# Kernel tuning notes

Hardware: AMD Instinct MI355X
Metric: run time of the kernel (lower is better)

The kernel has to match this reference:

```python
import jax, jax.numpy as jnp
import numpy as np

TEMPERATURE = 0.5
EPS = 1e-12  # torch F.normalize eps


def _l2_normalize(x, eps=EPS):
    n = jnp.linalg.norm(x, axis=1, keepdims=True)
    return x / jnp.maximum(n, eps)


def setup_inputs() -> dict:
    key = jax.random.key(0)
    k1, k2 = jax.random.split(key)
    B, D = 4096, 512
    return {
        "polyline_embs": jax.random.normal(k1, (B, D), dtype=jnp.float32),
        "c_embs": jax.random.normal(k2, (B, D), dtype=jnp.float32),
    }


def reference(polyline_embs, c_embs):
    b = polyline_embs.shape[0]
    # double-normalization in the original (F.normalize then cosine_similarity)
    # is idempotent on unit vectors, so sim = Z @ Z^T with Z unit-normalized.
    z = _l2_normalize(jnp.concatenate([polyline_embs, c_embs], axis=0))  # [2B, D]
    sim = z @ z.T  # [2B, 2B] cosine similarity
    # positives: diag offsets +B and -B
    idx = jnp.arange(b)
    sim_ij = sim[idx, idx + b]
    sim_ji = sim[idx + b, idx]
    positives = jnp.concatenate([sim_ij, sim_ji], axis=0)  # [2B]
    nominator = jnp.exp(positives / TEMPERATURE)
    mask = 1.0 - jnp.eye(2 * b, dtype=sim.dtype)
    denominator = jnp.sum(mask * jnp.exp(sim / TEMPERATURE), axis=1)  # [2B]
    all_losses = -jnp.log(nominator / denominator)
    return jnp.sum(all_losses) / (2 * b)
```

## Files before the change

### kernel.cpp

```cpp
#include <hip/hip_runtime.h>
#include <hip/hip_bf16.h>

#define B_ROWS 4096
#define D_DIM  512
#define N_ROWS 8192
#define BM 128
#define BN 128
#define BKB 128
#define NBLK (N_ROWS / BM)
#define NPAIR (NBLK * (NBLK + 1) / 2)

typedef float f32x4 __attribute__((ext_vector_type(4)));
typedef int   v4i   __attribute__((ext_vector_type(4)));
typedef int   v8i   __attribute__((ext_vector_type(8)));

__device__ __forceinline__ float dpp_xor1_add(float v) {
    return v + __int_as_float(__builtin_amdgcn_mov_dpp(
        __float_as_int(v), 0xB1, 0xf, 0xf, true));
}
__device__ __forceinline__ float dpp_xor2_add(float v) {
    return v + __int_as_float(__builtin_amdgcn_mov_dpp(
        __float_as_int(v), 0x4E, 0xf, 0xf, true));
}
__device__ __forceinline__ float dpp_ror4_add(float v) {
    return v + __int_as_float(__builtin_amdgcn_mov_dpp(
        __float_as_int(v), 0x124, 0xf, 0xf, true));
}
__device__ __forceinline__ float dpp_ror8_add(float v) {
    return v + __int_as_float(__builtin_amdgcn_mov_dpp(
        __float_as_int(v), 0x128, 0xf, 0xf, true));
}

__global__ __launch_bounds__(256) void prep_kernel(
    const float* __restrict__ poly, const float* __restrict__ cemb,
    unsigned char* __restrict__ Z, float* __restrict__ row_sum,
    float* __restrict__ pos, unsigned int* __restrict__ counter)
{
    const int wave = threadIdx.x >> 6;
    const int lane = threadIdx.x & 63;
    const int r = blockIdx.x * 4 + wave;

    const float4* prow = (const float4*)(poly + (size_t)r * D_DIM) + lane * 2;
    const float4* crow = (const float4*)(cemb + (size_t)r * D_DIM) + lane * 2;
    const float4 p0 = prow[0], p1 = prow[1];
    const float4 c0 = crow[0], c1 = crow[1];

    float ssp = p0.x*p0.x + p0.y*p0.y + p0.z*p0.z + p0.w*p0.w
              + p1.x*p1.x + p1.y*p1.y + p1.z*p1.z + p1.w*p1.w;
    float ssc = c0.x*c0.x + c0.y*c0.y + c0.z*c0.z + c0.w*c0.w
              + c1.x*c1.x + c1.y*c1.y + c1.z*c1.z + c1.w*c1.w;
    float dt  = p0.x*c0.x + p0.y*c0.y + p0.z*c0.z + p0.w*c0.w
              + p1.x*c1.x + p1.y*c1.y + p1.z*c1.z + p1.w*c1.w;

    #pragma unroll
    for (int m = 1; m < 64; m <<= 1) {
        ssp += __shfl_xor(ssp, m);
        ssc += __shfl_xor(ssc, m);
        dt  += __shfl_xor(dt,  m);
    }

    const float sp = 1.0f / fmaxf(sqrtf(ssp), 1e-12f);
    const float sc = 1.0f / fmaxf(sqrtf(ssc), 1e-12f);

    int2 zp, zc;
    zp.x = __builtin_amdgcn_cvt_pk_fp8_f32(p0.x*sp, p0.y*sp, 0, false)
         | (__builtin_amdgcn_cvt_pk_fp8_f32(p0.z*sp, p0.w*sp, 0, false) << 16);
    zp.y = __builtin_amdgcn_cvt_pk_fp8_f32(p1.x*sp, p1.y*sp, 0, false)
         | (__builtin_amdgcn_cvt_pk_fp8_f32(p1.z*sp, p1.w*sp, 0, false) << 16);
    zc.x = __builtin_amdgcn_cvt_pk_fp8_f32(c0.x*sc, c0.y*sc, 0, false)
         | (__builtin_amdgcn_cvt_pk_fp8_f32(c0.z*sc, c0.w*sc, 0, false) << 16);
    zc.y = __builtin_amdgcn_cvt_pk_fp8_f32(c1.x*sc, c1.y*sc, 0, false)
         | (__builtin_amdgcn_cvt_pk_fp8_f32(c1.z*sc, c1.w*sc, 0, false) << 16);

    *(int2*)(Z + (size_t)r * D_DIM + lane * 8)            = zp;
    *(int2*)(Z + (size_t)(r + B_ROWS) * D_DIM + lane * 8) = zc;

    if (lane == 0) {
        pos[r] = dt * sp * sc;
        row_sum[2 * r]     = 0.0f;
        row_sum[2 * r + 1] = 0.0f;
        if (r == 0) *counter = 0u;
    }
}

__global__ __launch_bounds__(512) void sim_kernel(
    const unsigned char* __restrict__ Z, float* __restrict__ row_sum,
    const float* __restrict__ pos, float* __restrict__ out,
    unsigned int* __restrict__ counter)
{
    __shared__ __align__(16) unsigned char As[BM * BKB];
    __shared__ __align__(16) unsigned char Bs[BN * BKB];
    __shared__ __align__(16) float rP[BM][4];
    __shared__ __align__(8)  float cP[BN][2];
    __shared__ unsigned int lastFlag;

    const int t0 = blockIdx.x;
    int bi = (int)((129.0f - sqrtf(16641.0f - 8.0f * (float)t0)) * 0.5f);
    #define CFN(b) ((b) * (129 - (b)) / 2)
    while (CFN(bi + 1) <= t0) ++bi;
    while (CFN(bi) > t0) --bi;
    const int bj = bi + (t0 - CFN(bi));
    #undef CFN
    const bool diag = (bi == bj);

    const int ibase = bi * BM;
    const int jbase = bj * BN;
    const int tid   = threadIdx.x;

    const int srow = tid >> 3;
    const int gchk = (tid & 7) ^ (srow & 7);

    const int wave = tid >> 6;
    const int lane = tid & 63;
    const int wi = (wave >> 2) * 64;
    const int wj = (wave & 3) * 32;
    const int quad = lane >> 4;
    const int c    = lane & 15;

    f32x4 acc[4][2] = {};

    const int sg0 = (((quad << 1)    ) ^ (c & 7)) * 16;
    const int sg1 = (((quad << 1) | 1) ^ (c & 7)) * 16;

    #pragma unroll 1
    for (int k0 = 0; k0 < D_DIM; k0 += BKB) {
        #pragma unroll
        for (int it = 0; it < 2; ++it) {
            const int row = it * 64 + srow;
            const unsigned char* ga = Z + (size_t)(ibase + row) * D_DIM + k0 + gchk * 16;
            __builtin_amdgcn_global_load_lds(
                (const __attribute__((address_space(1))) void*)ga,
                (__attribute__((address_space(3))) void*)(As + it * 8192 + tid * 16),
                16, 0, 0);
        }
        if (!diag) {
            #pragma unroll
            for (int it = 0; it < 2; ++it) {
                const int row = it * 64 + srow;
                const unsigned char* gb = Z + (size_t)(jbase + row) * D_DIM + k0 + gchk * 16;
                __builtin_amdgcn_global_load_lds(
                    (const __attribute__((address_space(1))) void*)gb,
                    (__attribute__((address_space(3))) void*)(Bs + it * 8192 + tid * 16),
                    16, 0, 0);
            }
        }
        __syncthreads();

        const unsigned char* bb = diag ? As : Bs;

        v8i bfr[2];
        #pragma unroll
        for (int tj = 0; tj < 2; ++tj) {
            const unsigned char* base = bb + (wj + tj * 16 + c) * BKB;
            const v4i lo = *(const v4i*)(base + sg0);
            const v4i hi = *(const v4i*)(base + sg1);
            bfr[tj] = __builtin_shufflevector(lo, hi, 0, 1, 2, 3, 4, 5, 6, 7);
        }
        #pragma unroll
        for (int ti = 0; ti < 4; ++ti) {
            const unsigned char* base = As + (wi + ti * 16 + c) * BKB;
            const v4i lo = *(const v4i*)(base + sg0);
            const v4i hi = *(const v4i*)(base + sg1);
            const v8i afr = __builtin_shufflevector(lo, hi, 0, 1, 2, 3, 4, 5, 6, 7);
            #pragma unroll
            for (int tj = 0; tj < 2; ++tj)
                acc[ti][tj] = __builtin_amdgcn_mfma_scale_f32_16x16x128_f8f6f4(
                    afr, bfr[tj], acc[ti][tj],
                    0, 0,
                    0, 0x7f7f7f7f,
                    0, 0x7f7f7f7f);
        }
        __syncthreads();
    }

    const float K2 = 2.885390081777927f;
    const int g = wave & 3;
    const int h = wave >> 2;
    float col[2] = {0.0f, 0.0f};

    #pragma unroll
    for (int ti = 0; ti < 4; ++ti) {
        const int li = wi + ti * 16 + quad * 4;
        #pragma unroll
        for (int r = 0; r < 4; ++r) {
            float v = 0.0f;
            if (diag) {
                const int gi = ibase + li + r;
                #pragma unroll
                for (int tj = 0; tj < 2; ++tj) {
                    const int gj = jbase + wj + tj * 16 + c;
                    const float e = (gj > gi) ? exp2f(K2 * acc[ti][tj][r]) : 0.0f;
                    v += e;
                    col[tj] += e;
                }
            } else {
                #pragma unroll
                for (int tj = 0; tj < 2; ++tj) {
                    const float e = exp2f(K2 * acc[ti][tj][r]);
                    v += e;
                    col[tj] += e;
                }
            }
            v = dpp_xor1_add(v);
            v = dpp_xor2_add(v);
            v = dpp_ror4_add(v);
            v = dpp_ror8_add(v);
            if (c == 0)
                rP[li + r][g] = v;
        }
    }
    #pragma unroll
    for (int tj = 0; tj < 2; ++tj) {
        float w = col[tj];
        w += __shfl_xor(w, 16);
        w += __shfl_xor(w, 32);
        if (quad == 0)
            cP[wj + tj * 16 + c][h] = w;
    }
    __syncthreads();

    if (tid < BM) {
        const float4 rp = *(const float4*)rP[tid];
        atomicAdd(&row_sum[ibase + tid], rp.x + rp.y + rp.z + rp.w);
    } else if (tid < 2 * BM) {
        const float2 cp = *(const float2*)cP[tid - BM];
        atomicAdd(&row_sum[jbase + tid - BM], cp.x + cp.y);
    }

    __syncthreads();
    if (tid == 0) {
        unsigned int old = __hip_atomic_fetch_add(
            counter, 1u, __ATOMIC_RELAXED, __HIP_MEMORY_SCOPE_AGENT);
        lastFlag = (old == NPAIR - 1) ? 1u : 0u;
    }
    __syncthreads();
    if (lastFlag) {
        float accL = 0.0f, accP = 0.0f;
        for (int i = tid; i < N_ROWS; i += 512) {
            const float rs = __hip_atomic_load(
                &row_sum[i], __ATOMIC_RELAXED, __HIP_MEMORY_SCOPE_AGENT);
            accL += __logf(rs);
        }
        for (int r = tid; r < B_ROWS; r += 512)
            accP += pos[r];
        #pragma unroll
        for (int m = 1; m < 64; m <<= 1) {
            accL += __shfl_xor(accL, m);
            accP += __shfl_xor(accP, m);
        }
        if (lane == 0) { rP[wave][0] = accL; rP[wave][1] = accP; }
        __syncthreads();
        if (tid == 0) {
            float L = 0.0f, P = 0.0f;
            #pragma unroll
            for (int w = 0; w < 8; ++w) { L += rP[w][0]; P += rP[w][1]; }
            out[0] = (L - 4.0f * P) / (float)N_ROWS;
        }
    }
}

extern "C" void kernel_launch(void* const* d_in, const int* in_sizes, int n_in,
                              void* d_out, int out_size, void* d_ws, size_t ws_size,
                              hipStream_t stream) {
    const float* poly = (const float*)d_in[0];
    const float* cemb = (const float*)d_in[1];

    unsigned char* Z       = (unsigned char*)d_ws;
    float*         row_sum = (float*)((char*)d_ws + (size_t)N_ROWS * D_DIM);
    float*         pos     = row_sum + N_ROWS;
    unsigned int*  counter = (unsigned int*)(pos + B_ROWS);
    float*         out     = (float*)d_out;

    prep_kernel<<<B_ROWS / 4, 256, 0, stream>>>(poly, cemb, Z, row_sum, pos, counter);
    sim_kernel<<<NPAIR, 512, 0, stream>>>(Z, row_sum, pos, out, counter);
}
```

Measured before the change: 115.8 us.

## Double-buffer LDS tiles to overlap global loads with MFMA compute

```diff
diff --git a/kernel.cpp b/kernel.cpp
--- a/kernel.cpp
+++ b/kernel.cpp
@@ -88,8 +88,8 @@
     const float* __restrict__ pos, float* __restrict__ out,
     unsigned int* __restrict__ counter)
 {
-    __shared__ __align__(16) unsigned char As[BM * BKB];
-    __shared__ __align__(16) unsigned char Bs[BN * BKB];
+    __shared__ __align__(16) unsigned char As[2][BM * BKB];
+    __shared__ __align__(16) unsigned char Bs[2][BN * BKB];
     __shared__ __align__(16) float rP[BM][4];
     __shared__ __align__(8)  float cP[BN][2];
     __shared__ unsigned int lastFlag;
@@ -122,15 +122,14 @@
     const int sg0 = (((quad << 1)    ) ^ (c & 7)) * 16;
     const int sg1 = (((quad << 1) | 1) ^ (c & 7)) * 16;
 
-    #pragma unroll 1
-    for (int k0 = 0; k0 < D_DIM; k0 += BKB) {
+    auto stage = [&](int buf, int k0) {
         #pragma unroll
         for (int it = 0; it < 2; ++it) {
             const int row = it * 64 + srow;
             const unsigned char* ga = Z + (size_t)(ibase + row) * D_DIM + k0 + gchk * 16;
             __builtin_amdgcn_global_load_lds(
                 (const __attribute__((address_space(1))) void*)ga,
-                (__attribute__((address_space(3))) void*)(As + it * 8192 + tid * 16),
+                (__attribute__((address_space(3))) void*)(&As[buf][it * 8192 + tid * 16]),
                 16, 0, 0);
         }
         if (!diag) {
@@ -140,13 +139,29 @@
                 const unsigned char* gb = Z + (size_t)(jbase + row) * D_DIM + k0 + gchk * 16;
                 __builtin_amdgcn_global_load_lds(
                     (const __attribute__((address_space(1))) void*)gb,
-                    (__attribute__((address_space(3))) void*)(Bs + it * 8192 + tid * 16),
+                    (__attribute__((address_space(3))) void*)(&Bs[buf][it * 8192 + tid * 16]),
                     16, 0, 0);
             }
         }
-        __syncthreads();
-
-        const unsigned char* bb = diag ? As : Bs;
+    };
+
+    stage(0, 0);
+
+    #pragma unroll 1
+    for (int t = 0; t < 4; ++t) {
+        if (t < 3) stage((t + 1) & 1, (t + 1) * BKB);
+
+        if (t < 3) {
+            if (diag) asm volatile("s_waitcnt vmcnt(2)" ::: "memory");
+            else      asm volatile("s_waitcnt vmcnt(4)" ::: "memory");
+        } else {
+            asm volatile("s_waitcnt vmcnt(0)" ::: "memory");
+        }
+        __builtin_amdgcn_s_barrier();
+        __builtin_amdgcn_sched_barrier(0);
+
+        const unsigned char* ab = As[t & 1];
+        const unsigned char* bb = diag ? ab : Bs[t & 1];
 
         v8i bfr[2];
         #pragma unroll
@@ -158,7 +173,7 @@
         }
         #pragma unroll
         for (int ti = 0; ti < 4; ++ti) {
-            const unsigned char* base = As + (wi + ti * 16 + c) * BKB;
+            const unsigned char* base = ab + (wi + ti * 16 + c) * BKB;
             const v4i lo = *(const v4i*)(base + sg0);
             const v4i hi = *(const v4i*)(base + sg1);
             const v8i afr = __builtin_shufflevector(lo, hi, 0, 1, 2, 3, 4, 5, 6, 7);
@@ -170,7 +185,9 @@
                     0, 0x7f7f7f7f,
                     0, 0x7f7f7f7f);
         }
-        __syncthreads();
+
+        asm volatile("s_waitcnt lgkmcnt(0)" ::: "memory");
+        __builtin_amdgcn_s_barrier();
     }
 
     const float K2 = 2.885390081777927f;
@@ -248,12 +265,12 @@
             accL += __shfl_xor(accL, m);
             accP += __shfl_xor(accP, m);
         }
-        if (lane == 0) { rP[wave][0] = accL; rP[wave][1] = accP; }
+        if (lane == 0) { rP[wave][0] = accL; cP[wave][0] = accP; }
         __syncthreads();
         if (tid == 0) {
             float L = 0.0f, P = 0.0f;
             #pragma unroll
-            for (int w = 0; w < 8; ++w) { L += rP[w][0]; P += rP[w][1]; }
+            for (int w = 0; w < 8; ++w) { L += rP[w][0]; P += cP[w][0]; }
             out[0] = (L - 4.0f * P) / (float)N_ROWS;
         }
     }
```

After: 114.6 us. About the same (-1.0%).
